# Performance work log

Measured on AMD Instinct MI355X. Metric: run time of the kernel, lower is better.

Reference implementation:

```python
import jax, jax.numpy as jnp
import numpy as np

H = 512          # hidden_size == input_size
K = 32768        # number of child cell inputs (lattice merge fan-in)


def setup_inputs() -> dict:
    key = jax.random.key(0)
    ks = jax.random.split(key, 8)
    s = 1.0 / np.sqrt(H)  # keep matmul outputs O(1)
    return {
        "input_": jax.random.normal(ks[0], (1, H), dtype=jnp.float32),
        "c_input": jax.random.normal(ks[1], (K, H), dtype=jnp.float32),
        "h_0": jax.random.normal(ks[2], (1, H), dtype=jnp.float32),
        "c_0": jax.random.normal(ks[3], (1, H), dtype=jnp.float32),
        "weight_ih": jax.random.normal(ks[4], (H, 3 * H), dtype=jnp.float32) * s,
        "weight_hh": jax.random.normal(ks[5], (H, 3 * H), dtype=jnp.float32) * s,
        "bias": jnp.zeros((3 * H,), dtype=jnp.float32),
        "alpha_weight_ih": jax.random.normal(ks[6], (H, H), dtype=jnp.float32) * s,
        "alpha_weight_hh": jax.random.normal(ks[7], (H, H), dtype=jnp.float32) * s,
    }


def reference(input_, c_input, h_0, c_0, weight_ih, weight_hh, bias,
              alpha_weight_ih, alpha_weight_hh):
    # Gate pre-activations: addmm(bias, h_0, W_hh) + input_ @ W_ih  -> [1, 3H]
    gates = h_0 @ weight_hh + bias + input_ @ weight_ih
    i, o, g = jnp.split(gates, 3, axis=1)        # each [1, H]
    i = jax.nn.sigmoid(i)
    o = jax.nn.sigmoid(o)
    g = jnp.tanh(g)

    # Variable-child softmax-weighted cell merge (non-empty c_input branch)
    alpha_wi = input_ @ alpha_weight_ih          # [1, H], broadcast over K
    alpha_wh = c_input @ alpha_weight_hh         # [K, H]
    alpha = jax.nn.sigmoid(alpha_wi + alpha_wh)  # [K, H]

    logits = jnp.concatenate([i, alpha], axis=0)  # [K+1, H]
    w = jnp.exp(logits)
    w = w / (w.sum(axis=0, keepdims=True) + 1e-12)

    merge = jnp.concatenate([g, c_input], axis=0)  # [K+1, H]
    c_1 = (merge * w).sum(axis=0, keepdims=True)   # [1, H]
    h_1 = o * jnp.tanh(c_1)                        # [1, H]
    return h_1, c_1
```

## Files before the change

kernel.cpp:

```cpp
#include <hip/hip_runtime.h>
#include <hip/hip_bf16.h>
#include <stdint.h>

#define Hdim 512
#define KC   32768

typedef __hip_bfloat16 bf16;
typedef __attribute__((ext_vector_type(8))) short short8;
typedef __attribute__((ext_vector_type(4))) float float4v;

__device__ __forceinline__ unsigned int pack_bf16_trunc(float e0, float e1) {
  union { float f; unsigned int u; } a, b;
  a.f = e0; b.f = e1;
  return __builtin_amdgcn_perm(b.u, a.u, 0x07060302u);
}

__device__ __forceinline__ unsigned long long pack64(float4v v) {
  return (unsigned long long)pack_bf16_trunc(v[0], v[1])
       | ((unsigned long long)pack_bf16_trunc(v[2], v[3]) << 32);
}

__global__ __launch_bounds__(256) void prep_wt_kernel(
    const float* __restrict__ input_, const float* __restrict__ h_0,
    const float* __restrict__ w_ih, const float* __restrict__ w_hh,
    const float* __restrict__ a_w_ih, const float* __restrict__ a_w_hh,
    float* __restrict__ gates, float* __restrict__ awi, bf16* __restrict__ wt) {
  __shared__ float sh[64 * 65];
  const int t = threadIdx.x;
  const int b = blockIdx.x;
  if (b < 32) {
    const int lane = t & 63, wv = t >> 6;
    float* h0s = sh;
    float* ins = sh + 512;
    float* red = sh + 1024;
    for (int i = t; i < 512; i += 256) { h0s[i] = h_0[i]; ins[i] = input_[i]; }
    __syncthreads();
    float acc = 0.f;
    if (b < 24) {
      const int j = b * 64 + lane;
      const float* whh = w_hh + j;
      const float* wih = w_ih + j;
#pragma unroll 16
      for (int i = 0; i < 128; ++i) {
        const int d = wv * 128 + i;
        acc += h0s[d] * whh[(size_t)d * 1536] + ins[d] * wih[(size_t)d * 1536];
      }
    } else {
      const int j = (b - 24) * 64 + lane;
      const float* wai = a_w_ih + j;
#pragma unroll 16
      for (int i = 0; i < 128; ++i) {
        const int d = wv * 128 + i;
        acc += ins[d] * wai[(size_t)d * Hdim];
      }
    }
    red[wv * 64 + lane] = acc;
    __syncthreads();
    if (t < 64) {
      float s = red[t] + red[64 + t] + red[128 + t] + red[192 + t];
      if (b < 24) gates[b * 64 + t] = s;
      else        awi[(b - 24) * 64 + t] = s;
    }
  } else {
    const int bb = b - 32;
    const int d0 = (bb & 7) * 64, h0 = (bb >> 3) * 64;
    const int tx = t & 63, tw = t >> 6;
    float (*tile)[65] = (float (*)[65])sh;
#pragma unroll
    for (int r = 0; r < 16; ++r) {
      const int row = r * 4 + tw;
      tile[row][tx] = a_w_hh[(size_t)(d0 + row) * Hdim + h0 + tx];
    }
    __syncthreads();
#pragma unroll
    for (int r = 0; r < 16; ++r) {
      const int row = r * 4 + tw;
      wt[(size_t)(h0 + row) * Hdim + d0 + tx] = __float2bfloat16(tile[tx][row]);
    }
  }
}

__global__ __launch_bounds__(256) void gemm_reduce_kernel(
    const float* __restrict__ c_input, const bf16* __restrict__ WT,
    const float* __restrict__ awi,
    float* __restrict__ pw, float* __restrict__ pwc) {
  __shared__ __align__(16) bf16 AsBuf[2][128 * 64];
  __shared__ __align__(16) bf16 BsBuf[2][128 * 64];
  __shared__ float red_w[2][128];
  __shared__ float red_wc[2][128];

  const int tid  = threadIdx.x;
  const int lane = tid & 63;
  const int wave = tid >> 6;
  const int wm   = wave & 1;
  const int wn   = wave >> 1;
  const int lm   = lane & 15;
  const int lq   = lane >> 4;

  const int id     = blockIdx.x;
  const int kk_idx = ((id >> 5) << 3) | (id & 7);
  const int h_idx  = (id >> 3) & 3;
  const int kk0 = kk_idx * 128;
  const int h0  = h_idx * 128;

  char* const As0 = (char*)AsBuf[0];
  char* const As1 = (char*)AsBuf[1];
  char* const Bs0 = (char*)BsBuf[0];
  char* const Bs1 = (char*)BsBuf[1];

  const int sub   = tid & 15;
  const int rbase = tid >> 4;
  const float* aglobS = c_input + (size_t)(kk0 + rbase) * Hdim + sub * 4;
  const int a_lds = rbase * 128 + (((sub >> 1) ^ (rbase & 7)) * 16) + (sub & 1) * 8;

  const int brow0 = wave * 8 + (lane >> 3);
  const int bg    = lane & 7;
  const bf16* bglobS = WT + (size_t)(h0 + brow0) * Hdim + bg * 8;
  const int b_lds = brow0 * 128 + ((bg ^ (lane >> 3)) * 16);

  float4v acc[4][4];
#pragma unroll
  for (int i = 0; i < 4; ++i)
#pragma unroll
    for (int j = 0; j < 4; ++j)
      acc[i][j] = (float4v){0.f, 0.f, 0.f, 0.f};

  {
    float4v ap[8]; short8 bp[4];
#pragma unroll
    for (int j = 0; j < 8; ++j)
      ap[j] = *(const float4v*)(aglobS + j * 16 * Hdim);
#pragma unroll
    for (int r = 0; r < 4; ++r)
      bp[r] = *(const short8*)(bglobS + (size_t)r * 32 * Hdim);
#pragma unroll
    for (int j = 0; j < 8; ++j)
      *(unsigned long long*)(As0 + j * 2048 + a_lds) = pack64(ap[j]);
#pragma unroll
    for (int r = 0; r < 4; ++r)
      *(short8*)(Bs0 + r * 4096 + b_lds) = bp[r];
  }
  __syncthreads();

#define GITER(T, RAs, RBs, WAs, WBs, NOT_LAST)                              \
  do {                                                                      \
    float4v ap[8]; short8 bp[4];                                            \
    if (NOT_LAST) {                                                         \
      const int dn = ((T) + 1) * 64;                                        \
      _Pragma("unroll")                                                     \
      for (int j = 0; j < 8; ++j)                                           \
        ap[j] = *(const float4v*)(aglobS + j * 16 * Hdim + dn);             \
      _Pragma("unroll")                                                     \
      for (int r = 0; r < 4; ++r)                                           \
        bp[r] = *(const short8*)(bglobS + (size_t)r * 32 * Hdim + dn);      \
    }                                                                       \
    __builtin_amdgcn_sched_barrier(0);   \
    _Pragma("unroll")                                                       \
    for (int ks = 0; ks < 2; ++ks) {                                        \
      short8 a[4], bfr[4];                                                  \
      _Pragma("unroll")                                                     \
      for (int mt = 0; mt < 4; ++mt) {                                      \
        const int row = wm * 64 + mt * 16 + lm;                             \
        a[mt] = *(const short8*)(RAs + row * 128 +                          \
                                 (((ks * 4 + lq) ^ (lm & 7)) * 16));        \
      }                                                                     \
      _Pragma("unroll")                                                     \
      for (int nt = 0; nt < 4; ++nt) {                                      \
        const int row = wn * 64 + nt * 16 + lm;                             \
        bfr[nt] = *(const short8*)(RBs + row * 128 +                        \
                                   (((ks * 4 + lq) ^ (lm & 7)) * 16));      \
      }                                                                     \
      _Pragma("unroll")                                                     \
      for (int mt = 0; mt < 4; ++mt)                                        \
        _Pragma("unroll")                                                   \
        for (int nt = 0; nt < 4; ++nt)                                      \
          acc[mt][nt] = __builtin_amdgcn_mfma_f32_16x16x32_bf16(            \
              a[mt], bfr[nt], acc[mt][nt], 0, 0, 0);                        \
    }                                                                       \
    if (NOT_LAST) {                                                         \
      _Pragma("unroll")                                                     \
      for (int j = 0; j < 8; ++j)                                           \
        *(unsigned long long*)(WAs + j * 2048 + a_lds) = pack64(ap[j]);     \
      _Pragma("unroll")                                                     \
      for (int r = 0; r < 4; ++r)                                           \
        *(short8*)(WBs + r * 4096 + b_lds) = bp[r];                         \
    }                                                                       \
    __syncthreads();                                                        \
  } while (0)

  GITER(0, As0, Bs0, As1, Bs1, 1);
  GITER(1, As1, Bs1, As0, Bs0, 1);
  GITER(2, As0, Bs0, As1, Bs1, 1);
  GITER(3, As1, Bs1, As0, Bs0, 1);
  GITER(4, As0, Bs0, As1, Bs1, 1);
  GITER(5, As1, Bs1, As0, Bs0, 1);
  GITER(6, As0, Bs0, As1, Bs1, 1);
  GITER(7, As1, Bs1, As0, Bs0, 0);
#undef GITER

  float awi_l[4];
#pragma unroll
  for (int nt = 0; nt < 4; ++nt)
    awi_l[nt] = awi[h0 + wn * 64 + nt * 16 + lm];

  float sw[4] = {0.f, 0.f, 0.f, 0.f}, swc[4] = {0.f, 0.f, 0.f, 0.f};
#pragma unroll
  for (int nt = 0; nt < 4; ++nt) {
    const int h = h0 + wn * 64 + nt * 16 + lm;
#pragma unroll
    for (int mt = 0; mt < 4; ++mt) {
      const int kkb = kk0 + wm * 64 + mt * 16 + lq * 4;
#pragma unroll
      for (int r = 0; r < 4; ++r) {
        float v = acc[mt][nt][r] + awi_l[nt];
        float aval = 1.f / (1.f + __expf(-v));
        float e = __expf(aval);
        float c = c_input[(size_t)(kkb + r) * Hdim + h];
        sw[nt]  += e;
        swc[nt] += e * c;
      }
    }
  }
#pragma unroll
  for (int nt = 0; nt < 4; ++nt) {
    sw[nt]  += __shfl_xor(sw[nt], 16, 64);
    sw[nt]  += __shfl_xor(sw[nt], 32, 64);
    swc[nt] += __shfl_xor(swc[nt], 16, 64);
    swc[nt] += __shfl_xor(swc[nt], 32, 64);
  }
  if (lq == 0) {
#pragma unroll
    for (int nt = 0; nt < 4; ++nt) {
      red_w[wm][wn * 64 + nt * 16 + lm]  = sw[nt];
      red_wc[wm][wn * 64 + nt * 16 + lm] = swc[nt];
    }
  }
  __syncthreads();
  if (tid < 128) {
    pw[(size_t)kk_idx * Hdim + h0 + tid]  = red_w[0][tid] + red_w[1][tid];
    pwc[(size_t)kk_idx * Hdim + h0 + tid] = red_wc[0][tid] + red_wc[1][tid];
  }
}

__global__ __launch_bounds__(256) void finalize_kernel(
    const float* __restrict__ pw, const float* __restrict__ pwc,
    const float* __restrict__ gates, const float* __restrict__ bias,
    float* __restrict__ out) {
  __shared__ float rsw[8][32], rswc[8][32];
  const int t = threadIdx.x;
  const int hl = t & 31, q = t >> 5;
  const int hh = blockIdx.x * 32 + hl;
  float sw = 0.f, swc = 0.f;
#pragma unroll 8
  for (int kb = q * 32; kb < q * 32 + 32; ++kb) {
    sw  += pw[(size_t)kb * Hdim + hh];
    swc += pwc[(size_t)kb * Hdim + hh];
  }
  rsw[q][hl] = sw; rswc[q][hl] = swc;
  __syncthreads();
  if (t < 32) {
    const int h = blockIdx.x * 32 + t;
    sw = 0.f; swc = 0.f;
#pragma unroll
    for (int q2 = 0; q2 < 8; ++q2) { sw += rsw[q2][t]; swc += rswc[q2][t]; }
    float ipre = gates[h] + bias[h];
    float opre = gates[Hdim + h] + bias[Hdim + h];
    float gpre = gates[2 * Hdim + h] + bias[2 * Hdim + h];
    float ei = expf(1.f / (1.f + expf(-ipre)));
    float g  = tanhf(gpre);
    float o  = 1.f / (1.f + expf(-opre));
    float denom = ei + sw + 1e-12f;
    float c1 = (ei * g + swc) / denom;
    float h1 = o * tanhf(c1);
    out[h]        = h1;
    out[Hdim + h] = c1;
  }
}

extern "C" void kernel_launch(void* const* d_in, const int* in_sizes, int n_in,
                              void* d_out, int out_size, void* d_ws, size_t ws_size,
                              hipStream_t stream) {
  const float* input_  = (const float*)d_in[0];
  const float* c_input = (const float*)d_in[1];
  const float* h_0     = (const float*)d_in[2];
  const float* w_ih    = (const float*)d_in[4];
  const float* w_hh    = (const float*)d_in[5];
  const float* bias    = (const float*)d_in[6];
  const float* a_w_ih  = (const float*)d_in[7];
  const float* a_w_hh  = (const float*)d_in[8];

  char* ws = (char*)d_ws;
  float* pw    = (float*)ws;
  float* pwc   = (float*)(ws + 512 * 1024);
  float* gates = (float*)(ws + 1024 * 1024);
  float* awi   = (float*)(ws + 1024 * 1024 + 6144);
  bf16*  WT    = (bf16*)(ws + 1024 * 1024 + 8192);

  hipLaunchKernelGGL(prep_wt_kernel, dim3(96), dim3(256), 0, stream,
                     input_, h_0, w_ih, w_hh, a_w_ih, a_w_hh, gates, awi, WT);
  hipLaunchKernelGGL(gemm_reduce_kernel, dim3(1024), dim3(256), 0, stream,
                     c_input, WT, awi, pw, pwc);
  hipLaunchKernelGGL(finalize_kernel, dim3(16), dim3(256), 0, stream,
                     pw, pwc, gates, bias, (float*)d_out);
}
```

Measured before the change: 147.3 us.

## Fuse finalize into GEMM kernel via atomics and last-block ticket

```diff
diff --git a/kernel.cpp b/kernel.cpp
--- a/kernel.cpp
+++ b/kernel.cpp
@@ -24,10 +24,16 @@
     const float* __restrict__ input_, const float* __restrict__ h_0,
     const float* __restrict__ w_ih, const float* __restrict__ w_hh,
     const float* __restrict__ a_w_ih, const float* __restrict__ a_w_hh,
-    float* __restrict__ gates, float* __restrict__ awi, bf16* __restrict__ wt) {
+    float* __restrict__ gates, float* __restrict__ awi, bf16* __restrict__ wt,
+    float* __restrict__ swg, float* __restrict__ swcg, int* __restrict__ counter) {
   __shared__ float sh[64 * 65];
   const int t = threadIdx.x;
   const int b = blockIdx.x;
+  if (b == 0) {
+    swg[t] = 0.f;  swg[256 + t] = 0.f;
+    swcg[t] = 0.f; swcg[256 + t] = 0.f;
+    if (t == 0) *counter = 0;
+  }
   if (b < 32) {
     const int lane = t & 63, wv = t >> 6;
     float* h0s = sh;
@@ -83,11 +89,14 @@
 __global__ __launch_bounds__(256) void gemm_reduce_kernel(
     const float* __restrict__ c_input, const bf16* __restrict__ WT,
     const float* __restrict__ awi,
-    float* __restrict__ pw, float* __restrict__ pwc) {
+    float* __restrict__ swg, float* __restrict__ swcg, int* __restrict__ counter,
+    const float* __restrict__ gates, const float* __restrict__ bias,
+    float* __restrict__ out) {
   __shared__ __align__(16) bf16 AsBuf[2][128 * 64];
   __shared__ __align__(16) bf16 BsBuf[2][128 * 64];
   __shared__ float red_w[2][128];
   __shared__ float red_wc[2][128];
+  __shared__ int ticket;
 
   const int tid  = threadIdx.x;
   const int lane = tid & 63;
@@ -237,43 +246,29 @@
   }
   __syncthreads();
   if (tid < 128) {
-    pw[(size_t)kk_idx * Hdim + h0 + tid]  = red_w[0][tid] + red_w[1][tid];
-    pwc[(size_t)kk_idx * Hdim + h0 + tid] = red_wc[0][tid] + red_wc[1][tid];
-  }
-}
-
-__global__ __launch_bounds__(256) void finalize_kernel(
-    const float* __restrict__ pw, const float* __restrict__ pwc,
-    const float* __restrict__ gates, const float* __restrict__ bias,
-    float* __restrict__ out) {
-  __shared__ float rsw[8][32], rswc[8][32];
-  const int t = threadIdx.x;
-  const int hl = t & 31, q = t >> 5;
-  const int hh = blockIdx.x * 32 + hl;
-  float sw = 0.f, swc = 0.f;
-#pragma unroll 8
-  for (int kb = q * 32; kb < q * 32 + 32; ++kb) {
-    sw  += pw[(size_t)kb * Hdim + hh];
-    swc += pwc[(size_t)kb * Hdim + hh];
-  }
-  rsw[q][hl] = sw; rswc[q][hl] = swc;
+    atomicAdd(&swg[h0 + tid],  red_w[0][tid] + red_w[1][tid]);
+    atomicAdd(&swcg[h0 + tid], red_wc[0][tid] + red_wc[1][tid]);
+  }
+  __threadfence();
   __syncthreads();
-  if (t < 32) {
-    const int h = blockIdx.x * 32 + t;
-    sw = 0.f; swc = 0.f;
-#pragma unroll
-    for (int q2 = 0; q2 < 8; ++q2) { sw += rsw[q2][t]; swc += rswc[q2][t]; }
-    float ipre = gates[h] + bias[h];
-    float opre = gates[Hdim + h] + bias[Hdim + h];
-    float gpre = gates[2 * Hdim + h] + bias[2 * Hdim + h];
-    float ei = expf(1.f / (1.f + expf(-ipre)));
-    float g  = tanhf(gpre);
-    float o  = 1.f / (1.f + expf(-opre));
-    float denom = ei + sw + 1e-12f;
-    float c1 = (ei * g + swc) / denom;
-    float h1 = o * tanhf(c1);
-    out[h]        = h1;
-    out[Hdim + h] = c1;
+  if (tid == 0) ticket = atomicAdd(counter, 1);
+  __syncthreads();
+  if (ticket == 1024 - 1) {
+    for (int h = tid; h < Hdim; h += 256) {
+      float swt  = atomicAdd(&swg[h], 0.f);
+      float swct = atomicAdd(&swcg[h], 0.f);
+      float ipre = gates[h] + bias[h];
+      float opre = gates[Hdim + h] + bias[Hdim + h];
+      float gpre = gates[2 * Hdim + h] + bias[2 * Hdim + h];
+      float ei = expf(1.f / (1.f + expf(-ipre)));
+      float g  = tanhf(gpre);
+      float o  = 1.f / (1.f + expf(-opre));
+      float denom = ei + swt + 1e-12f;
+      float c1 = (ei * g + swct) / denom;
+      float h1 = o * tanhf(c1);
+      out[h]        = h1;
+      out[Hdim + h] = c1;
+    }
   }
 }
 
@@ -290,16 +285,17 @@
   const float* a_w_hh  = (const float*)d_in[8];
 
   char* ws = (char*)d_ws;
-  float* pw    = (float*)ws;
-  float* pwc   = (float*)(ws + 512 * 1024);
-  float* gates = (float*)(ws + 1024 * 1024);
-  float* awi   = (float*)(ws + 1024 * 1024 + 6144);
-  bf16*  WT    = (bf16*)(ws + 1024 * 1024 + 8192);
+  float* swg     = (float*)ws;
+  float* swcg    = (float*)(ws + 2048);
+  int*   counter = (int*)(ws + 4096);
+  float* gates   = (float*)(ws + 8192);
+  float* awi     = (float*)(ws + 8192 + 6144);
+  bf16*  WT      = (bf16*)(ws + 16384);
 
   hipLaunchKernelGGL(prep_wt_kernel, dim3(96), dim3(256), 0, stream,
-                     input_, h_0, w_ih, w_hh, a_w_ih, a_w_hh, gates, awi, WT);
+                     input_, h_0, w_ih, w_hh, a_w_ih, a_w_hh, gates, awi, WT,
+                     swg, swcg, counter);
   hipLaunchKernelGGL(gemm_reduce_kernel, dim3(1024), dim3(256), 0, stream,
-                     c_input, WT, awi, pw, pwc);
-  hipLaunchKernelGGL(finalize_kernel, dim3(16), dim3(256), 0, stream,
-                     pw, pwc, gates, bias, (float*)d_out);
-}
+                     c_input, WT, awi, swg, swcg, counter, gates, bias,
+                     (float*)d_out);
+}
```

Measured after the change: 243.6 us. +65.4%, slower.
